# Performance work log

Measured on AMD Instinct MI355X. Metric: run time of the kernel, lower is better.

## Reference

```python
import jax, jax.numpy as jnp
import numpy as np

D_MODEL = 1024
NUM_HEADS = 16
D_K = D_MODEL // NUM_HEADS
THETA = 10000.0
B, S = 4, 2048


def _rope(x, theta=THETA):
    # x: [b, n, s, d_k]; interleaved pair rotation with base theta
    d = x.shape[-1]
    s = x.shape[-2]
    inv_freq = theta ** (-jnp.arange(0, d, 2, dtype=jnp.float32) / d)  # [d/2]
    pos = jnp.arange(s, dtype=jnp.float32)
    ang = pos[:, None] * inv_freq[None, :]          # [s, d/2]
    cos, sin = jnp.cos(ang), jnp.sin(ang)           # broadcast over b, n
    x1 = x[..., 0::2]
    x2 = x[..., 1::2]
    r1 = x1 * cos - x2 * sin
    r2 = x1 * sin + x2 * cos
    out = jnp.stack([r1, r2], axis=-1).reshape(x.shape)
    return out.astype(x.dtype)


def setup_inputs() -> dict:
    key = jax.random.key(0)
    ks = jax.random.split(key, 5)
    scale = 1.0 / np.sqrt(D_MODEL)
    return {
        "x": jax.random.normal(ks[0], (B, S, D_MODEL), dtype=jnp.float32),
        "W_q": jax.random.normal(ks[1], (D_MODEL, D_MODEL), dtype=jnp.float32) * scale,
        "W_k": jax.random.normal(ks[2], (D_MODEL, D_MODEL), dtype=jnp.float32) * scale,
        "W_v": jax.random.normal(ks[3], (D_MODEL, D_MODEL), dtype=jnp.float32) * scale,
        "W_o": jax.random.normal(ks[4], (D_MODEL, D_MODEL), dtype=jnp.float32) * scale,
    }


def reference(x, W_q, W_k, W_v, W_o):
    b, s, _ = x.shape
    # QKV projections (Linear stores weight as [out, in]; y = x @ W.T)
    q = jnp.einsum("bsd,ed->bse", x, W_q).reshape(b, s, NUM_HEADS, D_K).transpose(0, 2, 1, 3)
    k = jnp.einsum("bsd,ed->bse", x, W_k).reshape(b, s, NUM_HEADS, D_K).transpose(0, 2, 1, 3)
    v = jnp.einsum("bsd,ed->bse", x, W_v).reshape(b, s, NUM_HEADS, D_K).transpose(0, 2, 1, 3)
    q = _rope(q)
    k = _rope(k)
    scale = 1.0 / jnp.sqrt(jnp.asarray(D_K, dtype=x.dtype))
    scores = jnp.einsum("bnqd,bnkd->bnqk", q, k) * scale  # [b,n,s,s]
    causal = jnp.tril(jnp.ones((s, s), dtype=bool))
    scores = jnp.where(causal, scores, jnp.asarray(-jnp.inf, dtype=scores.dtype))
    attn = jax.nn.softmax(scores, axis=-1)
    out = jnp.einsum("bnqk,bnkd->bnqd", attn, v)          # [b,n,s,d_k]
    out = out.transpose(0, 2, 1, 3).reshape(b, s, D_MODEL)
    return jnp.einsum("bsd,ed->bse", out, W_o)
```

## Files before the change

kernel.cpp:

```cpp
#include <hip/hip_runtime.h>

#define AS1 __attribute__((address_space(1)))
#define AS3 __attribute__((address_space(3)))

typedef short short8 __attribute__((ext_vector_type(8)));
typedef float f32x4 __attribute__((ext_vector_type(4)));

#define DM 1024
#define NH 16
#define DKH 64
#define SEQ 2048
#define NB 4
#define ROWS (NB*SEQ)
#define QTILES (SEQ/128)

__device__ __forceinline__ unsigned short f2bf(float x) {
    union { float f; unsigned u; } v; v.f = x;
    unsigned r = v.u + 0x7fffu + ((v.u >> 16) & 1u);
    return (unsigned short)(r >> 16);
}
__device__ __forceinline__ float bf2f(unsigned short b) {
    union { unsigned u; float f; } v; v.u = ((unsigned)b) << 16;
    return v.f;
}
__device__ __forceinline__ unsigned cvtpk_bf16(float lo, float hi) {
    unsigned r;
    asm("v_cvt_pk_bf16_f32 %0, %1, %2" : "=v"(r) : "v"(lo), "v"(hi));
    return r;
}

__device__ __forceinline__ void gload_lds16(const void* g, void* l) {
    const AS1 unsigned int* gp = (const AS1 unsigned int*)(unsigned long long)g;
    AS3 unsigned int* lp = (AS3 unsigned int*)(unsigned)(unsigned long long)l;
    __builtin_amdgcn_global_load_lds(gp, lp, 16, 0, 0);
}

__device__ __forceinline__ f32x4 mfma_bf16(short8 a, short8 b, f32x4 c) {
    return __builtin_amdgcn_mfma_f32_16x16x32_bf16(a, b, c, 0, 0, 0);
}

__global__ void __launch_bounds__(256) prep_kernel(
    const float* __restrict__ x,
    const float* __restrict__ Wq, const float* __restrict__ Wk,
    const float* __restrict__ Wv, const float* __restrict__ Wo,
    unsigned short* __restrict__ xb, unsigned short* __restrict__ wbase,
    float2* __restrict__ tab) {
    int bid = blockIdx.x, tid = threadIdx.x;
    if (bid < 12288) {
        const float* src;
        unsigned short* dst;
        int i;
        if (bid < 8192) {
            src = x; dst = xb; i = bid * 256 + tid;
        } else {
            int id2 = bid - 8192;
            int w = id2 >> 10;
            src = w == 0 ? Wq : (w == 1 ? Wk : (w == 2 ? Wv : Wo));
            dst = wbase + (size_t)w * (1024 * 1024);
            i = (id2 & 1023) * 256 + tid;
        }
        float4 v = reinterpret_cast<const float4*>(src)[i];
        ushort4 o;
        o.x = f2bf(v.x); o.y = f2bf(v.y); o.z = f2bf(v.z); o.w = f2bf(v.w);
        reinterpret_cast<ushort4*>(dst)[i] = o;
    } else {
        int idx = (bid - 12288) * 256 + tid;
        int pos = idx >> 5, i = idx & 31;
        float inv = powf(10000.0f, -(float)i * (1.0f / 32.0f));
        float ang = (float)pos * inv;
        float2 cs; cs.x = cosf(ang); cs.y = sinf(ang);
        tab[idx] = cs;
    }
}

template <int STORE_F32>
__device__ __forceinline__ void gemm_bt_body(const unsigned short* __restrict__ A,
                                             const unsigned short* __restrict__ Bw,
                                             void* __restrict__ C, int m0, int n0,
                                             const float2* __restrict__ tab, float rs,
                                             unsigned short* __restrict__ vt, int outmode) {
    __shared__ unsigned short S[128 * 128];
    unsigned short* As = S;
    unsigned short* Bs = S + 128 * 64;
    const int tid = threadIdx.x;
    const int lane = tid & 63;
    const int wave = tid >> 6;
    const int wr = wave >> 1, wc = wave & 1;
    const int l15 = lane & 15, l4 = lane >> 4;

    f32x4 acc[4][4];
    #pragma unroll
    for (int m = 0; m < 4; ++m)
        #pragma unroll
        for (int n = 0; n < 4; ++n) { f32x4 z = {0.f, 0.f, 0.f, 0.f}; acc[m][n] = z; }

    const int srow = wave * 8 + (lane >> 3);
    const int gsw = (lane & 7) ^ (srow & 7);
    const unsigned short* Ag = A + (size_t)m0 * DM;
    const unsigned short* Bg = Bw + (size_t)n0 * DM;

    for (int kt = 0; kt < DM; kt += 64) {
        __syncthreads();
        #pragma unroll
        for (int it = 0; it < 4; ++it) {
            int row = it * 32 + srow;
            gload_lds16(Ag + (size_t)row * DM + kt + gsw * 8, (char*)As + (it * 4 + wave) * 1024);
            gload_lds16(Bg + (size_t)row * DM + kt + gsw * 8, (char*)Bs + (it * 4 + wave) * 1024);
        }
        __syncthreads();
        #pragma unroll
        for (int kc = 0; kc < 2; ++kc) {
            short8 af[4], bfr[4];
            #pragma unroll
            for (int m = 0; m < 4; ++m) {
                int row = 64 * wr + 16 * m + l15;
                int off = row * 128 + (((4 * kc + l4) ^ (row & 7)) << 4);
                af[m] = *(const short8*)((const char*)As + off);
            }
            #pragma unroll
            for (int n = 0; n < 4; ++n) {
                int row = 64 * wc + 16 * n + l15;
                int off = row * 128 + (((4 * kc + l4) ^ (row & 7)) << 4);
                bfr[n] = *(const short8*)((const char*)Bs + off);
            }
            #pragma unroll
            for (int m = 0; m < 4; ++m)
                #pragma unroll
                for (int n = 0; n < 4; ++n)
                    acc[m][n] = mfma_bf16(af[m], bfr[n], acc[m][n]);
        }
    }

    if (STORE_F32) {
        int rbase = m0 + 64 * wr + 4 * l4;
        int cbase = n0 + 64 * wc + l15;
        #pragma unroll
        for (int m = 0; m < 4; ++m)
            #pragma unroll
            for (int n = 0; n < 4; ++n) {
                int c = cbase + 16 * n;
                #pragma unroll
                for (int j = 0; j < 4; ++j)
                    ((float*)C)[(size_t)(rbase + 16 * m + j) * DM + c] = acc[m][n][j];
            }
    } else {
        __syncthreads();
        #pragma unroll
        for (int m = 0; m < 4; ++m) {
            int rb = 64 * wr + 16 * m + 4 * l4;
            int xr = ((rb >> 2) & 7) << 3;
            #pragma unroll
            for (int n = 0; n < 4; ++n) {
                int c = (64 * wc + 16 * n + l15) ^ xr;
                #pragma unroll
                for (int j = 0; j < 4; ++j)
                    S[(rb + j) * 128 + c] = f2bf(acc[m][n][j]);
            }
        }
        __syncthreads();
        if (outmode == 2) {
            int bidx = m0 >> 11;
            int stile = m0 & (SEQ - 1);
            int hA = n0 >> 6;
            unsigned short* vtb = vt + (size_t)(bidx * (NH * 64) + hA * 64) * SEQ;
            #pragma unroll
            for (int rep = 0; rep < 8; ++rep) {
                int idx = rep * 256 + tid;
                int vtrow = idx >> 4;
                int grp = idx & 15;
                int tg = grp >> 3, kg = grp & 7;
                int kc = kg >> 2, mq = kg & 3;
                short8 o;
                #pragma unroll
                for (int jj = 0; jj < 8; ++jj) {
                    int t = 32 * kc + 16 * (jj >> 2) + 4 * mq + (jj & 3);
                    int r = tg * 64 + t;
                    o[jj] = (short)S[r * 128 + (vtrow ^ (((r >> 2) & 7) << 3))];
                }
                *(short8*)(vtb + (size_t)vtrow * SEQ + stile + tg * 64 + kg * 8) = o;
            }
        } else {
            unsigned short* Cg = (unsigned short*)C + (size_t)m0 * DM + n0;
            #pragma unroll
            for (int r8 = 0; r8 < 8; ++r8) {
                int row = r8 * 16 + (tid >> 4);
                int oc = tid & 15;
                short8 v = *(const short8*)(S + row * 128 + ((oc ^ ((row >> 2) & 7)) << 3));
                if (rs > 0.f) {
                    int pos = (m0 + row) & (SEQ - 1);
                    const float2* tp = tab + pos * 32 + (oc & 7) * 4;
                    short8 o;
                    #pragma unroll
                    for (int tt = 0; tt < 4; ++tt) {
                        float cc = tp[tt].x * rs, ss = tp[tt].y * rs;
                        float e0 = bf2f((unsigned short)v[2 * tt]);
                        float e1 = bf2f((unsigned short)v[2 * tt + 1]);
                        o[2 * tt]     = (short)f2bf(e0 * cc - e1 * ss);
                        o[2 * tt + 1] = (short)f2bf(e0 * ss + e1 * cc);
                    }
                    v = o;
                }
                *(short8*)(Cg + (size_t)row * DM + oc * 8) = v;
            }
        }
    }
}

__global__ void __launch_bounds__(256) gemm_qkv_kernel(
    const unsigned short* __restrict__ X,
    const unsigned short* __restrict__ Wq, const unsigned short* __restrict__ Wk,
    const unsigned short* __restrict__ Wv,
    unsigned short* __restrict__ Qo, unsigned short* __restrict__ Ko,
    unsigned short* __restrict__ Vtg,
    const float2* __restrict__ tab) {
    int mt = blockIdx.x >> 3, nt = blockIdx.x & 7;
    int z = blockIdx.z;
    const unsigned short* W = z == 0 ? Wq : (z == 1 ? Wk : Wv);
    unsigned short* O = z == 0 ? Qo : Ko;
    gemm_bt_body<0>(X, W, O, mt * 128, nt * 128, tab,
                    z < 2 ? 1.0f : 0.f, Vtg, z == 2 ? 2 : 0);
}

__global__ void __launch_bounds__(256) gemm_out_kernel(
    const unsigned short* __restrict__ AO, const unsigned short* __restrict__ Wo,
    float* __restrict__ out) {
    int mt = blockIdx.x >> 3, nt = blockIdx.x & 7;
    gemm_bt_body<1>(AO, Wo, out, mt * 128, nt * 128, nullptr, 0.f, nullptr, 0);
}

template <int MODE>
__device__ __forceinline__ void attn_tile(const unsigned short* bufKV,
                                          const short8 (&aq)[2][2], f32x4 (&oacc)[2][4],
                                          float (&mrow)[2], float (&lrow)[2],
                                          int l15, int l4, int qloc) {
    const float CS = 0.125f * 1.44269504088896f;
    const char* bK = (const char*)bufKV;
    const char* bV = (const char*)bufKV + 8192;
    f32x4 sac[2][4];
    #pragma unroll
    for (int f = 0; f < 2; ++f)
        #pragma unroll
        for (int n = 0; n < 4; ++n) { f32x4 z = {0.f, 0.f, 0.f, 0.f}; sac[f][n] = z; }

    #pragma unroll
    for (int kc = 0; kc < 2; ++kc)
        #pragma unroll
        for (int n = 0; n < 4; ++n) {
            int row = 16 * n + l15;
            short8 ak = *(const short8*)(bK + row * 128 + (((4 * kc + l4) ^ (row & 7)) << 4));
            if (MODE < 2) sac[0][n] = mfma_bf16(ak, aq[0][kc], sac[0][n]);
            sac[1][n] = mfma_bf16(ak, aq[1][kc], sac[1][n]);
        }

    short8 pb[2][2];
    #pragma unroll
    for (int f = (MODE == 2 ? 1 : 0); f < 2; ++f) {
        const bool dg = (MODE == 1 && f == 0) || (MODE == 2);
        float sv[4][4];
        float tm = -1e30f;
        #pragma unroll
        for (int n = 0; n < 4; ++n)
            #pragma unroll
            for (int j = 0; j < 4; ++j) {
                float s = sac[f][n][j] * CS;
                if (dg && (16 * n + 4 * l4 + j) > qloc) s = -1e30f;
                sv[n][j] = s;
                tm = fmaxf(tm, s);
            }
        tm = fmaxf(tm, __shfl_xor(tm, 16, 64));
        tm = fmaxf(tm, __shfl_xor(tm, 32, 64));
        float nm = fmaxf(mrow[f], tm);
        float al = exp2f(mrow[f] - nm);
        mrow[f] = nm;
        float pj[4][4];
        float sum = 0.f;
        #pragma unroll
        for (int n = 0; n < 4; ++n)
            #pragma unroll
            for (int j = 0; j < 4; ++j) {
                float p = exp2f(sv[n][j] - nm);
                pj[n][j] = p; sum += p;
            }
        sum += __shfl_xor(sum, 16, 64);
        sum += __shfl_xor(sum, 32, 64);
        lrow[f] = lrow[f] * al + sum;
        #pragma unroll
        for (int n = 0; n < 4; ++n) oacc[f][n] *= al;
        #pragma unroll
        for (int kc = 0; kc < 2; ++kc) {
            union { unsigned u[4]; short8 s8; } P;
            P.u[0] = cvtpk_bf16(pj[2 * kc][0], pj[2 * kc][1]);
            P.u[1] = cvtpk_bf16(pj[2 * kc][2], pj[2 * kc][3]);
            P.u[2] = cvtpk_bf16(pj[2 * kc + 1][0], pj[2 * kc + 1][1]);
            P.u[3] = cvtpk_bf16(pj[2 * kc + 1][2], pj[2 * kc + 1][3]);
            pb[f][kc] = P.s8;
        }
    }

    #pragma unroll
    for (int kc = 0; kc < 2; ++kc)
        #pragma unroll
        for (int n = 0; n < 4; ++n) {
            int row = 16 * n + l15;
            short8 av = *(const short8*)(bV + row * 128 + (((4 * kc + l4) ^ (row & 7)) << 4));
            if (MODE < 2) oacc[0][n] = mfma_bf16(av, pb[0][kc], oacc[0][n]);
            oacc[1][n] = mfma_bf16(av, pb[1][kc], oacc[1][n]);
        }
}

__global__ void __launch_bounds__(256) attn_kernel(const unsigned short* __restrict__ Q,
                                                   const unsigned short* __restrict__ K,
                                                   const unsigned short* __restrict__ Vtg,
                                                   unsigned short* __restrict__ O) {
    __shared__ unsigned short smem[9216];

    const int tid = threadIdx.x, lane = tid & 63, wave = tid >> 6;
    const int l15 = lane & 15, l4 = lane >> 4;
    const int bh = blockIdx.x;
    const int yg = blockIdx.y >> 2, yl = blockIdx.y & 3;
    const int qt = yg == 0 ? 15 - yl : (yg == 1 ? yl : (yg == 2 ? 11 - yl : 4 + yl));
    const int b = bh >> 4, h = bh & 15;
    const size_t base = (size_t)b * SEQ * DM + (size_t)h * DKH;
    const unsigned short* Qb = Q + base;
    const unsigned short* Kb = K + base;
    const unsigned short* Vg = Vtg + (size_t)bh * 64 * SEQ;
    unsigned short* Ob = O + base;

    const int q0 = qt * 128;
    const int qloc = 16 * wave + l15;
    const int NT = 2 * qt + 2;

    short8 aq[2][2];
    #pragma unroll
    for (int f = 0; f < 2; ++f) {
        const unsigned short* p = Qb + (size_t)(q0 + 64 * f + 16 * wave + l15) * DM + 8 * l4;
        aq[f][0] = *(const short8*)p;
        aq[f][1] = *(const short8*)(p + 32);
    }

    f32x4 oacc[2][4];
    #pragma unroll
    for (int f = 0; f < 2; ++f)
        #pragma unroll
        for (int n = 0; n < 4; ++n) { f32x4 z = {0.f, 0.f, 0.f, 0.f}; oacc[f][n] = z; }
    float mrow[2] = {-1e30f, -1e30f};
    float lrow[2] = {0.f, 0.f};

    const int srow = wave * 8 + (lane >> 3);
    const int gsw = (lane & 7) ^ (srow & 7);
    const unsigned short* kp = Kb + (size_t)srow * DM + gsw * 8;
    const unsigned short* vp = Vg + (size_t)srow * SEQ + gsw * 8;
    unsigned short* s0 = smem + ((0 * 4 + wave) * 1024 + lane * 16) / 2;
    unsigned short* s1 = smem + ((1 * 4 + wave) * 1024 + lane * 16) / 2;
    unsigned short* s2 = smem + (8192 + (0 * 4 + wave) * 1024 + lane * 16) / 2;
    unsigned short* s3 = smem + (8192 + (1 * 4 + wave) * 1024 + lane * 16) / 2;

    short8 rk0 = *(const short8*)(kp);
    short8 rk1 = *(const short8*)(kp + 32 * DM);
    short8 rv0 = *(const short8*)(vp);
    short8 rv1 = *(const short8*)(vp + 32 * SEQ);
    kp += 64 * DM; vp += 64;
    *(short8*)s0 = rk0; *(short8*)s1 = rk1;
    *(short8*)s2 = rv0; *(short8*)s3 = rv1;
    __syncthreads();

    for (int t = 0; t < NT; ++t) {
        if (t + 1 < NT) {
            rk0 = *(const short8*)(kp);
            rk1 = *(const short8*)(kp + 32 * DM);
            rv0 = *(const short8*)(vp);
            rv1 = *(const short8*)(vp + 32 * SEQ);
            kp += 64 * DM; vp += 64;
        }
        if (t < NT - 2)       attn_tile<0>(smem, aq, oacc, mrow, lrow, l15, l4, qloc);
        else if (t == NT - 2) attn_tile<1>(smem, aq, oacc, mrow, lrow, l15, l4, qloc);
        else                  attn_tile<2>(smem, aq, oacc, mrow, lrow, l15, l4, qloc);
        __syncthreads();
        if (t + 1 < NT) {
            *(short8*)s0 = rk0; *(short8*)s1 = rk1;
            *(short8*)s2 = rv0; *(short8*)s3 = rv1;
            __syncthreads();
        }
    }

    unsigned short* ep = smem + wave * 2304;
    float inv[2] = {1.f / lrow[0], 1.f / lrow[1]};
    #pragma unroll
    for (int f = 0; f < 2; ++f)
        #pragma unroll
        for (int n = 0; n < 4; ++n)
            #pragma unroll
            for (int j = 0; j < 4; ++j)
                ep[(f * 16 + l15) * 72 + 16 * n + 4 * l4 + j] = f2bf(oacc[f][n][j] * inv[f]);
    __syncthreads();
    #pragma unroll
    for (int i = 0; i < 4; ++i) {
        int r = i * 8 + (lane >> 3), cg = lane & 7;
        int grow = q0 + 64 * (r >> 4) + 16 * wave + (r & 15);
        *(short8*)(Ob + (size_t)grow * DM + cg * 8) = *(const short8*)(ep + r * 72 + cg * 8);
    }
}

extern "C" void kernel_launch(void* const* d_in, const int* in_sizes, int n_in,
                              void* d_out, int out_size, void* d_ws, size_t ws_size,
                              hipStream_t stream) {
    (void)in_sizes; (void)n_in; (void)out_size; (void)ws_size;
    const float* x  = (const float*)d_in[0];
    const float* Wq = (const float*)d_in[1];
    const float* Wk = (const float*)d_in[2];
    const float* Wv = (const float*)d_in[3];
    const float* Wo = (const float*)d_in[4];
    float* out = (float*)d_out;

    char* ws = (char*)d_ws;
    const size_t MB = 1024 * 1024;
    unsigned short* xb  = (unsigned short*)(ws);
    unsigned short* wqb = (unsigned short*)(ws + 16 * MB);
    unsigned short* wkb = (unsigned short*)(ws + 18 * MB);
    unsigned short* wvb = (unsigned short*)(ws + 20 * MB);
    unsigned short* wob = (unsigned short*)(ws + 22 * MB);
    unsigned short* Qb  = (unsigned short*)(ws + 24 * MB);
    unsigned short* Kb  = (unsigned short*)(ws + 40 * MB);
    unsigned short* Vtg = (unsigned short*)(ws + 56 * MB);
    unsigned short* AO  = (unsigned short*)(ws + 72 * MB);
    float2* tab = (float2*)(ws + 88 * MB);

    prep_kernel<<<12544, 256, 0, stream>>>(x, Wq, Wk, Wv, Wo, xb, wqb, tab);
    gemm_qkv_kernel<<<dim3(512, 1, 3), 256, 0, stream>>>(xb, wqb, wkb, wvb, Qb, Kb, Vtg, tab);
    attn_kernel<<<dim3(NB * NH, QTILES), 256, 0, stream>>>(Qb, Kb, Vtg, AO);
    gemm_out_kernel<<<512, 256, 0, stream>>>(AO, wob, out);
}
```

Measured before the change: 215.0 us.

## Double-buffer attention K/V LDS tiles and remap GEMM block order per XCD

The attention kernel now uses two LDS buffers for K/V tiles. The next tile is written into the alternate buffer right after the current tile is computed, which drops one __syncthreads per iteration. Both GEMM kernels now remap blockIdx so that consecutive blocks, which are spread round-robin across the 8 XCDs, land on the same XCD and share row tiles of X/AO and weight tiles in L2. The QKV GEMM also flattens its grid from z=3 to a single dimension. The risk is the doubled LDS footprint (32KB), which may lower attention occupancy.

```diff
diff --git a/kernel.cpp b/kernel.cpp
--- a/kernel.cpp
+++ b/kernel.cpp
@@ -213,8 +213,11 @@
     unsigned short* __restrict__ Qo, unsigned short* __restrict__ Ko,
     unsigned short* __restrict__ Vtg,
     const float2* __restrict__ tab) {
-    int mt = blockIdx.x >> 3, nt = blockIdx.x & 7;
-    int z = blockIdx.z;
+    int o = blockIdx.x;
+    int v = (o & 7) * 192 + (o >> 3);
+    int mt = v / 24;
+    int c = v - mt * 24;
+    int z = c >> 3, nt = c & 7;
     const unsigned short* W = z == 0 ? Wq : (z == 1 ? Wk : Wv);
     unsigned short* O = z == 0 ? Qo : Ko;
     gemm_bt_body<0>(X, W, O, mt * 128, nt * 128, tab,
@@ -224,7 +227,9 @@
 __global__ void __launch_bounds__(256) gemm_out_kernel(
     const unsigned short* __restrict__ AO, const unsigned short* __restrict__ Wo,
     float* __restrict__ out) {
-    int mt = blockIdx.x >> 3, nt = blockIdx.x & 7;
+    int o = blockIdx.x;
+    int v = (o & 7) * 64 + (o >> 3);
+    int mt = v >> 3, nt = v & 7;
     gemm_bt_body<1>(AO, Wo, out, mt * 128, nt * 128, nullptr, 0.f, nullptr, 0);
 }
 
@@ -312,7 +317,7 @@
                                                    const unsigned short* __restrict__ K,
                                                    const unsigned short* __restrict__ Vtg,
                                                    unsigned short* __restrict__ O) {
-    __shared__ unsigned short smem[9216];
+    __shared__ unsigned short smem[16384];
 
     const int tid = threadIdx.x, lane = tid & 63, wave = tid >> 6;
     const int l15 = lane & 15, l4 = lane >> 4;
@@ -350,37 +355,39 @@
     const int gsw = (lane & 7) ^ (srow & 7);
     const unsigned short* kp = Kb + (size_t)srow * DM + gsw * 8;
     const unsigned short* vp = Vg + (size_t)srow * SEQ + gsw * 8;
-    unsigned short* s0 = smem + ((0 * 4 + wave) * 1024 + lane * 16) / 2;
-    unsigned short* s1 = smem + ((1 * 4 + wave) * 1024 + lane * 16) / 2;
-    unsigned short* s2 = smem + (8192 + (0 * 4 + wave) * 1024 + lane * 16) / 2;
-    unsigned short* s3 = smem + (8192 + (1 * 4 + wave) * 1024 + lane * 16) / 2;
+    const int c0 = ((0 * 4 + wave) * 1024 + lane * 16) / 2;
+    const int c1 = ((1 * 4 + wave) * 1024 + lane * 16) / 2;
+    const int c2 = (8192 + (0 * 4 + wave) * 1024 + lane * 16) / 2;
+    const int c3 = (8192 + (1 * 4 + wave) * 1024 + lane * 16) / 2;
 
     short8 rk0 = *(const short8*)(kp);
     short8 rk1 = *(const short8*)(kp + 32 * DM);
     short8 rv0 = *(const short8*)(vp);
     short8 rv1 = *(const short8*)(vp + 32 * SEQ);
     kp += 64 * DM; vp += 64;
-    *(short8*)s0 = rk0; *(short8*)s1 = rk1;
-    *(short8*)s2 = rv0; *(short8*)s3 = rv1;
+    *(short8*)(smem + c0) = rk0; *(short8*)(smem + c1) = rk1;
+    *(short8*)(smem + c2) = rv0; *(short8*)(smem + c3) = rv1;
     __syncthreads();
 
     for (int t = 0; t < NT; ++t) {
-        if (t + 1 < NT) {
+        const bool pre = (t + 1 < NT);
+        if (pre) {
             rk0 = *(const short8*)(kp);
             rk1 = *(const short8*)(kp + 32 * DM);
             rv0 = *(const short8*)(vp);
             rv1 = *(const short8*)(vp + 32 * SEQ);
             kp += 64 * DM; vp += 64;
         }
-        if (t < NT - 2)       attn_tile<0>(smem, aq, oacc, mrow, lrow, l15, l4, qloc);
-        else if (t == NT - 2) attn_tile<1>(smem, aq, oacc, mrow, lrow, l15, l4, qloc);
-        else                  attn_tile<2>(smem, aq, oacc, mrow, lrow, l15, l4, qloc);
+        const unsigned short* buf = smem + (t & 1) * 8192;
+        if (t < NT - 2)       attn_tile<0>(buf, aq, oacc, mrow, lrow, l15, l4, qloc);
+        else if (t == NT - 2) attn_tile<1>(buf, aq, oacc, mrow, lrow, l15, l4, qloc);
+        else                  attn_tile<2>(buf, aq, oacc, mrow, lrow, l15, l4, qloc);
+        if (pre) {
+            unsigned short* db = smem + ((t + 1) & 1) * 8192;
+            *(short8*)(db + c0) = rk0; *(short8*)(db + c1) = rk1;
+            *(short8*)(db + c2) = rv0; *(short8*)(db + c3) = rv1;
+        }
         __syncthreads();
-        if (t + 1 < NT) {
-            *(short8*)s0 = rk0; *(short8*)s1 = rk1;
-            *(short8*)s2 = rv0; *(short8*)s3 = rv1;
-            __syncthreads();
-        }
     }
 
     unsigned short* ep = smem + wave * 2304;
@@ -426,7 +433,7 @@
     float2* tab = (float2*)(ws + 88 * MB);
 
     prep_kernel<<<12544, 256, 0, stream>>>(x, Wq, Wk, Wv, Wo, xb, wqb, tab);
-    gemm_qkv_kernel<<<dim3(512, 1, 3), 256, 0, stream>>>(xb, wqb, wkb, wvb, Qb, Kb, Vtg, tab);
+    gemm_qkv_kernel<<<1536, 256, 0, stream>>>(xb, wqb, wkb, wvb, Qb, Kb, Vtg, tab);
     attn_kernel<<<dim3(NB * NH, QTILES), 256, 0, stream>>>(Qb, Kb, Vtg, AO);
     gemm_out_kernel<<<512, 256, 0, stream>>>(AO, wob, out);
 }
```

Measured after the change: 204.1 us. 1.05x faster.
